# Kernel tuning notes

Hardware: AMD Instinct MI355X
Metric: run time of the kernel (lower is better)

Reference implementation:

```python
import jax, jax.numpy as jnp
import numpy as np

N_NODES = 100000
N_EDGES = 1600000
F_IN = 64
HEADS = 2
D_HEAD = 64  # hidden_channels per head
F_OUT = HEADS * D_HEAD  # 128 (concat=True)
NEG_SLOPE = 0.2


def setup_inputs() -> dict:
    key = jax.random.key(0)
    ks = jax.random.split(key, 10)
    x = jax.random.normal(ks[0], (N_NODES, F_IN), dtype=jnp.float32)
    edge_index = jax.random.randint(ks[1], (2, N_EDGES), 0, N_NODES, dtype=jnp.int32)
    perm = jax.random.permutation(ks[2], N_NODES).astype(jnp.int32)
    s = 0.05
    W_src = jax.random.normal(ks[3], (F_IN, F_OUT), dtype=jnp.float32) * s
    W_dst = jax.random.normal(ks[4], (F_IN, F_OUT), dtype=jnp.float32) * s
    a_src = jax.random.normal(ks[5], (HEADS, D_HEAD), dtype=jnp.float32) * s
    a_dst = jax.random.normal(ks[6], (HEADS, D_HEAD), dtype=jnp.float32) * s
    bias = jnp.zeros((F_OUT,), dtype=jnp.float32)
    prelu_w = jnp.full((F_OUT,), 0.25, dtype=jnp.float32)  # torch PReLU default init
    return {"x": x, "edge_index": edge_index, "perm": perm,
            "W_src": W_src, "W_dst": W_dst, "a_src": a_src, "a_dst": a_dst,
            "bias": bias, "prelu_w": prelu_w}


def _gat_prelu(x, edge_index, W_src, W_dst, a_src, a_dst, bias, prelu_w):
    # PyG GATConv, add_self_loops=False, heads=HEADS, concat=True, then PReLU.
    N = x.shape[0]
    src, dst = edge_index[0], edge_index[1]
    xs = (x @ W_src).reshape(N, HEADS, D_HEAD)  # source-side projection
    xd = (x @ W_dst).reshape(N, HEADS, D_HEAD)  # destination-side projection
    al_s = jnp.einsum('nhd,hd->nh', xs, a_src)  # [N,H]
    al_d = jnp.einsum('nhd,hd->nh', xd, a_dst)  # [N,H]
    e = jax.nn.leaky_relu(al_s[src] + al_d[dst], NEG_SLOPE)  # [E,H]
    # softmax over incoming edges of each destination node
    m = jax.ops.segment_max(e, dst, num_segments=N)  # [N,H]
    ex = jnp.exp(e - m[dst])
    den = jax.ops.segment_sum(ex, dst, num_segments=N)  # [N,H]
    alpha = ex / (den[dst] + 1e-16)  # [E,H]
    msg = xs[src] * alpha[:, :, None]  # [E,H,D]
    out = jax.ops.segment_sum(msg, dst, num_segments=N)  # [N,H,D]
    out = out.reshape(N, F_OUT) + bias
    return jnp.where(out >= 0, out, prelu_w * out)


def reference(x, edge_index, perm, W_src, W_dst, a_src, a_dst, bias, prelu_w):
    # DGI forward: positive embedding, corrupted (negative) embedding, summary
    pos_z = _gat_prelu(x, edge_index, W_src, W_dst, a_src, a_dst, bias, prelu_w)
    x_cor = x[perm]  # corruption: permute node features, keep edges
    neg_z = _gat_prelu(x_cor, edge_index, W_src, W_dst, a_src, a_dst, bias, prelu_w)
    summary = jax.nn.sigmoid(pos_z.mean(axis=0))
    return pos_z, neg_z, summary
```

## Files before the change

### kernel.cpp

```cpp
#include <hip/hip_runtime.h>
#include <hip/hip_bf16.h>

#define F_IN   64
#define HEADS  2
#define D_HEAD 64
#define F_OUT  128
#define NEG_SLOPE 0.2f

#define AGG_GRID 2048
#define CAP 48

__device__ __forceinline__ float bf_lo(unsigned v) { return __uint_as_float((v & 0xffffu) << 16); }
__device__ __forceinline__ float bf_hi(unsigned v) { return __uint_as_float(v & 0xffff0000u); }

__global__ __launch_bounds__(256, 2) void proj_kernel(
    const float* __restrict__ x, const float* __restrict__ W,
    const float* __restrict__ Wd,
    const float* __restrict__ as_, const float* __restrict__ ad_,
    __hip_bfloat16* __restrict__ xsb, float* __restrict__ als, float* __restrict__ ald,
    int* __restrict__ cnt, int N)
{
    __shared__ float xsh[8][64];
    __shared__ float a2dsh[128];
    int t = threadIdx.x;
    int c    = t & 127;
    int slot = t >> 7;
    int h    = c >> 6;
    int j    = c & 63;

    for (int g = blockIdx.x * 256 + t; g < N + 128; g += gridDim.x * 256) cnt[g] = 0;

    float Wcol[64];
    #pragma unroll
    for (int k = 0; k < 64; ++k) Wcol[k] = W[k * 128 + c];

    if (t < 128) {
        int jj = t >> 1, hh = t & 1;
        float sd = 0.f;
        #pragma unroll 8
        for (int d = 0; d < 64; ++d) sd += Wd[jj * 128 + hh * 64 + d] * ad_[hh * 64 + d];
        a2dsh[t] = sd;
    }

    float asv = as_[h * 64 + j];

    for (long long base = (long long)blockIdx.x * 8; base < N; base += (long long)gridDim.x * 8) {
        __syncthreads();
        {
            int r  = t >> 5;
            int kk = (t & 31) * 2;
            long long nn = base + r;
            float2 v = (nn < N) ? *reinterpret_cast<const float2*>(x + nn * 64 + kk)
                                : make_float2(0.f, 0.f);
            xsh[r][kk]     = v.x;
            xsh[r][kk + 1] = v.y;
        }
        __syncthreads();

        float acc0 = 0.f, acc1 = 0.f, acc2 = 0.f, acc3 = 0.f;
        #pragma unroll
        for (int k4 = 0; k4 < 64; k4 += 4) {
            float4 x0 = *reinterpret_cast<const float4*>(&xsh[slot    ][k4]);
            float4 x1 = *reinterpret_cast<const float4*>(&xsh[slot + 2][k4]);
            float4 x2 = *reinterpret_cast<const float4*>(&xsh[slot + 4][k4]);
            float4 x3 = *reinterpret_cast<const float4*>(&xsh[slot + 6][k4]);
            acc0 += x0.x * Wcol[k4] + x0.y * Wcol[k4+1] + x0.z * Wcol[k4+2] + x0.w * Wcol[k4+3];
            acc1 += x1.x * Wcol[k4] + x1.y * Wcol[k4+1] + x1.z * Wcol[k4+2] + x1.w * Wcol[k4+3];
            acc2 += x2.x * Wcol[k4] + x2.y * Wcol[k4+1] + x2.z * Wcol[k4+2] + x2.w * Wcol[k4+3];
            acc3 += x3.x * Wcol[k4] + x3.y * Wcol[k4+1] + x3.z * Wcol[k4+2] + x3.w * Wcol[k4+3];
        }

        float a2dv = a2dsh[j * 2 + h];
        float rs0 = acc0 * asv, rd0 = xsh[slot    ][j] * a2dv;
        float rs1 = acc1 * asv, rd1 = xsh[slot + 2][j] * a2dv;
        float rs2 = acc2 * asv, rd2 = xsh[slot + 4][j] * a2dv;
        float rs3 = acc3 * asv, rd3 = xsh[slot + 6][j] * a2dv;
        #pragma unroll
        for (int off = 32; off; off >>= 1) {
            rs0 += __shfl_down(rs0, off, 64); rd0 += __shfl_down(rd0, off, 64);
            rs1 += __shfl_down(rs1, off, 64); rd1 += __shfl_down(rd1, off, 64);
            rs2 += __shfl_down(rs2, off, 64); rd2 += __shfl_down(rd2, off, 64);
            rs3 += __shfl_down(rs3, off, 64); rd3 += __shfl_down(rd3, off, 64);
        }

        long long n0 = base + slot;
        if (n0     < N) xsb[(n0    ) * 128 + c] = __float2bfloat16(acc0);
        if (n0 + 2 < N) xsb[(n0 + 2) * 128 + c] = __float2bfloat16(acc1);
        if (n0 + 4 < N) xsb[(n0 + 4) * 128 + c] = __float2bfloat16(acc2);
        if (n0 + 6 < N) xsb[(n0 + 6) * 128 + c] = __float2bfloat16(acc3);
        if (j == 0) {
            if (n0     < N) { als[(n0    ) * 2 + h] = rs0; ald[(n0    ) * 2 + h] = rd0; }
            if (n0 + 2 < N) { als[(n0 + 2) * 2 + h] = rs1; ald[(n0 + 2) * 2 + h] = rd1; }
            if (n0 + 4 < N) { als[(n0 + 4) * 2 + h] = rs2; ald[(n0 + 4) * 2 + h] = rd2; }
            if (n0 + 6 < N) { als[(n0 + 6) * 2 + h] = rs3; ald[(n0 + 6) * 2 + h] = rd3; }
        }
    }
}

__global__ void scatter_kernel(const int2* __restrict__ src2, const int2* __restrict__ dst2,
                               const int* __restrict__ perm,
                               int* __restrict__ cnt, int2* __restrict__ csr2, int E2) {
    int i = blockIdx.x * blockDim.x + threadIdx.x;
    if (i >= E2) return;
    int2 s = src2[i];
    int2 d = dst2[i];
    int slot0 = atomicAdd(&cnt[d.x], 1);
    if (slot0 < CAP) csr2[d.x * CAP + slot0] = make_int2(s.x, perm[s.x]);
    int slot1 = atomicAdd(&cnt[d.y], 1);
    if (slot1 < CAP) csr2[d.y * CAP + slot1] = make_int2(s.y, perm[s.y]);
}

#define SHFL8(wArr, pArr, spv, wv, i)                      \
    _Pragma("unroll")                                      \
    for (int k = 0; k < 8; ++k) {                          \
        wArr[k] = __shfl(wv, hb + (i) + k, 64);            \
        pArr[k] = __shfl(spv, (i) + k, 64);                \
    }
#define LOAD8(vArr, pArr)                                  \
    _Pragma("unroll")                                      \
    for (int k = 0; k < 8; ++k) vArr[k] = xsu[pArr[k] * 64 + lane];
#define FMA8(a0, a1, wArr, vArr)                           \
    _Pragma("unroll")                                      \
    for (int k = 0; k < 8; ++k) {                          \
        a0 += wArr[k] * bf_lo(vArr[k]);                    \
        a1 += wArr[k] * bf_hi(vArr[k]);                    \
    }

__global__ __launch_bounds__(256, 4) void aggfused_kernel(
    const int* __restrict__ cnt,
    const int2* __restrict__ csr2,
    const int* __restrict__ perm,
    const float* __restrict__ als, const float* __restrict__ ald,
    const unsigned* __restrict__ xsu,
    const float* __restrict__ bias, const float* __restrict__ pw,
    float* __restrict__ zP, float* __restrict__ zN,
    float* __restrict__ colsum, int N)
{
    const int STEP = AGG_GRID * 4;
    int t    = threadIdx.x;
    int wid  = t >> 6;
    int lane = t & 63;
    int col  = lane * 2;
    int h    = lane >> 5;
    int rel  = lane & 31;
    int hb   = h << 5;
    float bi0 = bias[col], bi1 = bias[col + 1];
    float pw0 = pw[col],   pw1 = pw[col + 1];
    float sum0 = 0.f, sum1 = 0.f;

    const int NP = (N + 1) >> 1;
    int g0 = blockIdx.x * 4 + wid;

    int cA_c = 0, cB_c = 0;
    float aPA_c = 0.f, aNA_c = 0.f, aPB_c = 0.f, aNB_c = 0.f;
    if (g0 < NP) {
        int nA = g0 * 2, nB = nA + 1;
        cA_c = min(cnt[nA], CAP);
        aPA_c = ald[nA * 2 + h];
        aNA_c = ald[perm[nA] * 2 + h];
        if (nB < N) {
            cB_c = min(cnt[nB], CAP);
            aPB_c = ald[nB * 2 + h];
            aNB_c = ald[perm[nB] * 2 + h];
        }
    }

    for (int g = g0; g < NP; g += STEP) {
        int g2 = g + STEP;
        int cA_n = 0, cB_n = 0;
        float aPA_n = 0.f, aNA_n = 0.f, aPB_n = 0.f, aNB_n = 0.f;
        if (g2 < NP) {
            int nA2 = g2 * 2, nB2 = nA2 + 1;
            cA_n = min(cnt[nA2], CAP);
            aPA_n = ald[nA2 * 2 + h];
            aNA_n = ald[perm[nA2] * 2 + h];
            if (nB2 < N) {
                cB_n = min(cnt[nB2], CAP);
                aPB_n = ald[nB2 * 2 + h];
                aNB_n = ald[perm[nB2] * 2 + h];
            }
        }

        int nA = g * 2, nB = nA + 1;
        int cA = cA_c, cB = cB_c;
        long long eA = (long long)nA * CAP, eB = (long long)nB * CAP;

        float denPA = 0.f, aPA0 = 0.f, aPA1 = 0.f, denNA = 0.f, aNA0 = 0.f, aNA1 = 0.f;
        float denPB = 0.f, aPB0 = 0.f, aPB1 = 0.f, denNB = 0.f, aNB0 = 0.f, aNB1 = 0.f;

        float wPA = 0.f, wNA = 0.f, wPB = 0.f, wNB = 0.f;
        int spPA = 0, spNA = 0, spPB = 0, spNB = 0;

        int cmax = max(cA, cB);
        for (int rbase = 0; rbase < cmax; rbase += 32) {
            if (rbase < cA) {
                int o = rbase + rel;
                bool v = o < cA;
                long long raw = __builtin_nontemporal_load(
                    (const long long*)(csr2 + (v ? eA + o : eA)));
                spPA = v ? (int)(unsigned)(raw & 0xffffffffLL) : 0;
                spNA = v ? (int)(raw >> 32) : 0;
                float scP = als[spPA * 2 + h] + aPA_c;
                float scN = als[spNA * 2 + h] + aNA_c;
                scP = (scP >= 0.f) ? scP : NEG_SLOPE * scP;
                scN = (scN >= 0.f) ? scN : NEG_SLOPE * scN;
                wPA = v ? __expf(fminf(scP, 60.f)) : 0.f;
                wNA = v ? __expf(fminf(scN, 60.f)) : 0.f;
                denPA += wPA; denNA += wNA;
            }
            if (rbase < cB) {
                int o = rbase + rel;
                bool v = o < cB;
                long long raw = __builtin_nontemporal_load(
                    (const long long*)(csr2 + (v ? eB + o : eB)));
                spPB = v ? (int)(unsigned)(raw & 0xffffffffLL) : 0;
                spNB = v ? (int)(raw >> 32) : 0;
                float scP = als[spPB * 2 + h] + aPB_c;
                float scN = als[spNB * 2 + h] + aNB_c;
                scP = (scP >= 0.f) ? scP : NEG_SLOPE * scP;
                scN = (scN >= 0.f) ? scN : NEG_SLOPE * scN;
                wPB = v ? __expf(fminf(scP, 60.f)) : 0.f;
                wNB = v ? __expf(fminf(scN, 60.f)) : 0.f;
                denPB += wPB; denNB += wNB;
            }

            int ecA = min(32, cA - rbase);
            int ecB = min(32, cB - rbase);
            for (int i = 0; i < 32; i += 8) {
                bool doA = i < ecA, doB = i < ecB;
                if (doA && doB) {
                    float wpa[8], wna[8], wpb[8], wnb[8];
                    int   ppa[8], pna[8], ppb[8], pnb[8];
                    unsigned vpa[8], vna[8], vpb[8], vnb[8];
                    SHFL8(wpa, ppa, spPA, wPA, i); SHFL8(wna, pna, spNA, wNA, i);
                    SHFL8(wpb, ppb, spPB, wPB, i); SHFL8(wnb, pnb, spNB, wNB, i);
                    LOAD8(vpa, ppa); LOAD8(vna, pna); LOAD8(vpb, ppb); LOAD8(vnb, pnb);
                    FMA8(aPA0, aPA1, wpa, vpa); FMA8(aNA0, aNA1, wna, vna);
                    FMA8(aPB0, aPB1, wpb, vpb); FMA8(aNB0, aNB1, wnb, vnb);
                } else if (doA) {
                    float wpa[8], wna[8]; int ppa[8], pna[8]; unsigned vpa[8], vna[8];
                    SHFL8(wpa, ppa, spPA, wPA, i); SHFL8(wna, pna, spNA, wNA, i);
                    LOAD8(vpa, ppa); LOAD8(vna, pna);
                    FMA8(aPA0, aPA1, wpa, vpa); FMA8(aNA0, aNA1, wna, vna);
                } else if (doB) {
                    float wpb[8], wnb[8]; int ppb[8], pnb[8]; unsigned vpb[8], vnb[8];
                    SHFL8(wpb, ppb, spPB, wPB, i); SHFL8(wnb, pnb, spNB, wNB, i);
                    LOAD8(vpb, ppb); LOAD8(vnb, pnb);
                    FMA8(aPB0, aPB1, wpb, vpb); FMA8(aNB0, aNB1, wnb, vnb);
                } else {
                    break;
                }
            }
        }

        #pragma unroll
        for (int off = 16; off; off >>= 1) {
            denPA += __shfl_xor(denPA, off, 64);
            denNA += __shfl_xor(denNA, off, 64);
            denPB += __shfl_xor(denPB, off, 64);
            denNB += __shfl_xor(denNB, off, 64);
        }

        {
            float inv = 1.f / (denPA + 1e-16f);
            float v0 = aPA0 * inv + bi0, v1 = aPA1 * inv + bi1;
            v0 = (v0 >= 0.f) ? v0 : pw0 * v0;
            v1 = (v1 >= 0.f) ? v1 : pw1 * v1;
            float2 v2 = make_float2(v0, v1);
            __builtin_nontemporal_store(*(const double*)&v2,
                                        (double*)(zP + (long long)nA * 128 + col));
            sum0 += v0; sum1 += v1;
            inv = 1.f / (denNA + 1e-16f);
            v0 = aNA0 * inv + bi0; v1 = aNA1 * inv + bi1;
            v0 = (v0 >= 0.f) ? v0 : pw0 * v0;
            v1 = (v1 >= 0.f) ? v1 : pw1 * v1;
            v2 = make_float2(v0, v1);
            __builtin_nontemporal_store(*(const double*)&v2,
                                        (double*)(zN + (long long)nA * 128 + col));
        }
        if (nB < N) {
            float inv = 1.f / (denPB + 1e-16f);
            float v0 = aPB0 * inv + bi0, v1 = aPB1 * inv + bi1;
            v0 = (v0 >= 0.f) ? v0 : pw0 * v0;
            v1 = (v1 >= 0.f) ? v1 : pw1 * v1;
            float2 v2 = make_float2(v0, v1);
            __builtin_nontemporal_store(*(const double*)&v2,
                                        (double*)(zP + (long long)nB * 128 + col));
            sum0 += v0; sum1 += v1;
            inv = 1.f / (denNB + 1e-16f);
            v0 = aNB0 * inv + bi0; v1 = aNB1 * inv + bi1;
            v0 = (v0 >= 0.f) ? v0 : pw0 * v0;
            v1 = (v1 >= 0.f) ? v1 : pw1 * v1;
            v2 = make_float2(v0, v1);
            __builtin_nontemporal_store(*(const double*)&v2,
                                        (double*)(zN + (long long)nB * 128 + col));
        }

        cA_c = cA_n; cB_c = cB_n;
        aPA_c = aPA_n; aNA_c = aNA_n; aPB_c = aPB_n; aNB_c = aNB_n;
    }

    __shared__ float sh[512];
    sh[t * 2]     = sum0;
    sh[t * 2 + 1] = sum1;
    __syncthreads();
    if (wid == 0) {
        float s0 = sh[t * 2]     + sh[(t + 64) * 2]     + sh[(t + 128) * 2]     + sh[(t + 192) * 2];
        float s1 = sh[t * 2 + 1] + sh[(t + 64) * 2 + 1] + sh[(t + 128) * 2 + 1] + sh[(t + 192) * 2 + 1];
        atomicAdd(&colsum[col],     s0);
        atomicAdd(&colsum[col + 1], s1);
    }
}

__global__ void summary_kernel(const float* __restrict__ colsum, float* __restrict__ out,
                               float invN)
{
    int c = threadIdx.x;
    float m = colsum[c] * invN;
    out[c] = 1.f / (1.f + expf(-m));
}

extern "C" void kernel_launch(void* const* d_in, const int* in_sizes, int n_in,
                              void* d_out, int out_size, void* d_ws, size_t ws_size,
                              hipStream_t stream) {
    const float* x      = (const float*)d_in[0];
    const int*   ei     = (const int*)  d_in[1];
    const int*   perm   = (const int*)  d_in[2];
    const float* Wsrc   = (const float*)d_in[3];
    const float* Wdst   = (const float*)d_in[4];
    const float* a_src  = (const float*)d_in[5];
    const float* a_dst  = (const float*)d_in[6];
    const float* bias   = (const float*)d_in[7];
    const float* prelu  = (const float*)d_in[8];

    const int N = in_sizes[0] / F_IN;
    const int E = in_sizes[1] / 2;
    const int* src = ei;
    const int* dst = ei + E;

    float* ws = (float*)d_ws;
    long long off = 0;
    float* als    = ws + off; off += 2LL * N;
    float* ald    = ws + off; off += 2LL * N;
    int*   cnt    = (int*)(ws + off); off += N;
    float* colsum = ws + off; off += 128;
    int2*  csr2   = (int2*)(ws + off); off += 2LL * N * CAP;
    unsigned* xsu = (unsigned*)(ws + off); off += (long long)N * 64;

    float* outP = (float*)d_out;
    float* outN = outP + (long long)N * F_OUT;
    float* outS = outN + (long long)N * F_OUT;

    proj_kernel<<<1024, 256, 0, stream>>>(x, Wsrc, Wdst, a_src, a_dst,
                                          (__hip_bfloat16*)xsu, als, ald, cnt, N);

    const int E2 = E / 2;
    const int eb2 = (E2 + 255) / 256;
    scatter_kernel<<<eb2, 256, 0, stream>>>((const int2*)src, (const int2*)dst, perm,
                                            cnt, csr2, E2);

    aggfused_kernel<<<AGG_GRID, 256, 0, stream>>>(cnt, csr2, perm, als, ald, xsu,
                                                  bias, prelu, outP, outN, colsum, N);

    summary_kernel<<<1, 128, 0, stream>>>(colsum, outS, 1.0f / (float)N);
}
```

Before: 355.3 us.

## Fuse projection and edge scatter into one interleaved kernel launch

```diff
diff --git a/kernel.cpp b/kernel.cpp
--- a/kernel.cpp
+++ b/kernel.cpp
@@ -9,26 +9,51 @@
 
 #define AGG_GRID 2048
 #define CAP 48
+#define PROJ_BLOCKS 1024
 
 __device__ __forceinline__ float bf_lo(unsigned v) { return __uint_as_float((v & 0xffffu) << 16); }
 __device__ __forceinline__ float bf_hi(unsigned v) { return __uint_as_float(v & 0xffff0000u); }
 
-__global__ __launch_bounds__(256, 2) void proj_kernel(
+__global__ void zero_i(int* __restrict__ p, int n) {
+    int i = blockIdx.x * blockDim.x + threadIdx.x;
+    int step = gridDim.x * blockDim.x;
+    for (; i < n; i += step) p[i] = 0;
+}
+
+__global__ __launch_bounds__(256) void fusedps_kernel(
     const float* __restrict__ x, const float* __restrict__ W,
     const float* __restrict__ Wd,
     const float* __restrict__ as_, const float* __restrict__ ad_,
     __hip_bfloat16* __restrict__ xsb, float* __restrict__ als, float* __restrict__ ald,
-    int* __restrict__ cnt, int N)
+    int N,
+    const int2* __restrict__ src2, const int2* __restrict__ dst2,
+    const int* __restrict__ perm,
+    int* __restrict__ cnt, int2* __restrict__ csr2, int E2)
 {
+    int bid = blockIdx.x;
+    int q = bid >> 2, r = bid & 3;
+    bool is_proj = (r == 0) && (q < PROJ_BLOCKS);
+    int t = threadIdx.x;
+
+    if (!is_proj) {
+        int scat_bid = bid - min(q + (r > 0 ? 1 : 0), PROJ_BLOCKS);
+        int i = scat_bid * 256 + t;
+        if (i >= E2) return;
+        int2 s = src2[i];
+        int2 d = dst2[i];
+        int slot0 = atomicAdd(&cnt[d.x], 1);
+        if (slot0 < CAP) csr2[d.x * CAP + slot0] = make_int2(s.x, perm[s.x]);
+        int slot1 = atomicAdd(&cnt[d.y], 1);
+        if (slot1 < CAP) csr2[d.y * CAP + slot1] = make_int2(s.y, perm[s.y]);
+        return;
+    }
+
     __shared__ float xsh[8][64];
     __shared__ float a2dsh[128];
-    int t = threadIdx.x;
     int c    = t & 127;
     int slot = t >> 7;
     int h    = c >> 6;
     int j    = c & 63;
-
-    for (int g = blockIdx.x * 256 + t; g < N + 128; g += gridDim.x * 256) cnt[g] = 0;
 
     float Wcol[64];
     #pragma unroll
@@ -44,16 +69,16 @@
 
     float asv = as_[h * 64 + j];
 
-    for (long long base = (long long)blockIdx.x * 8; base < N; base += (long long)gridDim.x * 8) {
+    for (long long base = (long long)q * 8; base < N; base += (long long)PROJ_BLOCKS * 8) {
         __syncthreads();
         {
-            int r  = t >> 5;
+            int rr = t >> 5;
             int kk = (t & 31) * 2;
-            long long nn = base + r;
+            long long nn = base + rr;
             float2 v = (nn < N) ? *reinterpret_cast<const float2*>(x + nn * 64 + kk)
                                 : make_float2(0.f, 0.f);
-            xsh[r][kk]     = v.x;
-            xsh[r][kk + 1] = v.y;
+            xsh[rr][kk]     = v.x;
+            xsh[rr][kk + 1] = v.y;
         }
         __syncthreads();
 
@@ -95,19 +120,6 @@
             if (n0 + 6 < N) { als[(n0 + 6) * 2 + h] = rs3; ald[(n0 + 6) * 2 + h] = rd3; }
         }
     }
-}
-
-__global__ void scatter_kernel(const int2* __restrict__ src2, const int2* __restrict__ dst2,
-                               const int* __restrict__ perm,
-                               int* __restrict__ cnt, int2* __restrict__ csr2, int E2) {
-    int i = blockIdx.x * blockDim.x + threadIdx.x;
-    if (i >= E2) return;
-    int2 s = src2[i];
-    int2 d = dst2[i];
-    int slot0 = atomicAdd(&cnt[d.x], 1);
-    if (slot0 < CAP) csr2[d.x * CAP + slot0] = make_int2(s.x, perm[s.x]);
-    int slot1 = atomicAdd(&cnt[d.y], 1);
-    if (slot1 < CAP) csr2[d.y * CAP + slot1] = make_int2(s.y, perm[s.y]);
 }
 
 #define SHFL8(wArr, pArr, spv, wv, i)                      \
@@ -351,13 +363,14 @@
     float* outN = outP + (long long)N * F_OUT;
     float* outS = outN + (long long)N * F_OUT;
 
-    proj_kernel<<<1024, 256, 0, stream>>>(x, Wsrc, Wdst, a_src, a_dst,
-                                          (__hip_bfloat16*)xsu, als, ald, cnt, N);
+    zero_i<<<256, 256, 0, stream>>>(cnt, N + 128);
 
     const int E2 = E / 2;
     const int eb2 = (E2 + 255) / 256;
-    scatter_kernel<<<eb2, 256, 0, stream>>>((const int2*)src, (const int2*)dst, perm,
-                                            cnt, csr2, E2);
+    const int total_blocks = PROJ_BLOCKS + eb2;
+    fusedps_kernel<<<total_blocks, 256, 0, stream>>>(
+        x, Wsrc, Wdst, a_src, a_dst, (__hip_bfloat16*)xsu, als, ald, N,
+        (const int2*)src, (const int2*)dst, perm, cnt, csr2, E2);
 
     aggfused_kernel<<<AGG_GRID, 256, 0, stream>>>(cnt, csr2, perm, als, ald, xsu,
                                                   bias, prelu, outP, outN, colsum, N);
```

After: 405.1 us. +14.0%, slower.
